# Kernel optimization log

Measured on AMD Instinct MI355X. Metric: run time of the kernel, lower is better.

Reference implementation:

```python
import jax, jax.numpy as jnp
import numpy as np

B = 1024
D = 64          # embed_dim (symp == dise)
H1, H2 = 8, 8   # dsd metapath fanouts
U1, U2, U3 = 8, 8, 16  # usu metapath fanouts
NUM_SYMP = 50000
NUM_DISE = 2000
NEG_SLOPE = 0.2


def setup_inputs() -> dict:
    key = jax.random.key(0)
    ks = jax.random.split(key, 16)
    s = 0.05
    E_s = jax.random.normal(ks[0], (NUM_SYMP + 1, D), jnp.float32) * s
    E_d = jax.random.normal(ks[1], (NUM_DISE + 1, D), jnp.float32) * s
    # padding_idx=0 rows are zero in torch Embedding
    E_s = E_s.at[0].set(0.0)
    E_d = E_d.at[0].set(0.0)
    W = lambda k: jax.random.normal(k, (D, D), jnp.float32) * (1.0 / np.sqrt(D))
    return {
        "E_s": E_s,
        "E_d": E_d,
        "W_dsd_21": W(ks[2]),
        "W_dsd_22": W(ks[3]),
        "W_dsd_11": W(ks[4]),
        "W_dsd_12": W(ks[5]),
        "W_usu_3": W(ks[6]),
        "W_usu_21": W(ks[7]),
        "W_usu_22": W(ks[8]),
        "W_usu_1": W(ks[9]),
        "label": jax.random.randint(ks[10], (B,), 0, NUM_DISE + 1),
        "dsd_1": jax.random.randint(ks[11], (B, H1), 0, NUM_SYMP + 1),
        "dsd_2": jax.random.randint(ks[12], (B, H1, H2), 0, NUM_DISE + 1),
        "usu_1": jax.random.randint(ks[13], (B, U1), 0, NUM_SYMP + 1),
        "usu_2": jax.random.randint(ks[14], (B, U1, U2), 0, 10000),
        "usu_3": jax.random.randint(ks[15], (B, U1, U2, U3), 0, NUM_SYMP + 1),
    }


def _avg_real(msg, idx):
    # mean over the neighbor axis, counting only nonzero (real) neighbors;
    # zero output if all neighbors are padding (matches weight==1e8 -> 0)
    cnt = (idx != 0).sum(-1).astype(msg.dtype)
    w = jnp.where(cnt > 0, 1.0 / (cnt + 1e-8), 0.0)
    return msg.sum(-2) * w[..., None]


def _leaky(x):
    return jax.nn.leaky_relu(x, NEG_SLOPE)


def reference(E_s, E_d, W_dsd_21, W_dsd_22, W_dsd_11, W_dsd_12,
              W_usu_3, W_usu_21, W_usu_22, W_usu_1,
              label, dsd_1, dsd_2, usu_1, usu_2, usu_3):
    # ---- forward_dsd (eval mode: dropout = identity) ----
    td = E_d[label]                       # [B, D]
    es = E_s[dsd_1]                       # [B, H1, D]
    ed = E_d[dsd_2]                       # [B, H1, H2, D]
    m_sd = ed @ W_dsd_21.T + (ed * es[:, :, None, :]) @ W_dsd_22.T
    m_sd = _avg_real(m_sd, dsd_2)         # [B, H1, D]
    m_ss = es @ W_dsd_21.T                # [B, H1, D]
    emb_s1 = _leaky(m_ss + m_sd)          # [B, H1, D]
    m_ds = emb_s1 @ W_dsd_11.T + (emb_s1 * td[:, None, :]) @ W_dsd_12.T
    m_ds = _avg_real(m_ds, dsd_1)         # [B, D]
    emb_dise = _leaky(m_ds + td @ W_dsd_11.T)

    # ---- forward_usu ----
    u1 = E_s[usu_1]                       # [B, U1, D]
    s3 = E_s[usu_3]                       # [B, U1, U2, U3, D]
    m_us3 = _avg_real(s3 @ W_usu_3.T, usu_3)   # [B, U1, U2, D]
    eu2 = _leaky(m_us3)                   # [B, U1, U2, D]
    m_su = eu2 @ W_usu_21.T + (eu2 * u1[:, :, None, :]) @ W_usu_22.T
    m_su = _avg_real(m_su, usu_2)         # [B, U1, D]
    m_ss_u = u1 @ W_usu_21.T              # [B, U1, D]
    es1 = _leaky(m_ss_u + m_su)           # [B, U1, D]
    emb_user = _leaky(_avg_real(es1 @ W_usu_1.T, usu_1))  # [B, D]

    pred_score = (emb_dise * emb_user).sum(-1)  # [B]
    return pred_score
```

## Files before the change

kernel.cpp:

```cpp
#include <hip/hip_runtime.h>
#include <hip/hip_bf16.h>


typedef __attribute__((ext_vector_type(8))) short short8;
typedef __attribute__((ext_vector_type(8))) unsigned short ushort8;
typedef __attribute__((ext_vector_type(4))) float f32x4;

__device__ __forceinline__ int rfl(int v) { return __builtin_amdgcn_readfirstlane(v); }
__device__ __forceinline__ float bcastf(float v, int l) {
    return __int_as_float(__builtin_amdgcn_readlane(__float_as_int(v), l));
}
__device__ __forceinline__ float leakyf(float x) { return x >= 0.f ? x : 0.2f * x; }

__device__ __forceinline__ unsigned short bf16bits(float x) {
    __hip_bfloat16 h = __float2bfloat16(x);
    return __builtin_bit_cast(unsigned short, h);
}
__device__ __forceinline__ float bflo(unsigned int u) { return __uint_as_float(u << 16); }
__device__ __forceinline__ float bfhi(unsigned int u) { return __uint_as_float(u & 0xffff0000u); }

__device__ __forceinline__ void stage_w512(float* dst, const float* __restrict__ W, int tid) {
#pragma unroll
    for (int c = 0; c < 2; ++c) {
        int f4 = c * 512 + tid;
        int j = f4 >> 4, g = f4 & 15;
        float4 v = reinterpret_cast<const float4*>(W)[f4];
        reinterpret_cast<float4*>(dst)[(j << 4) + ((g + j) & 15)] = v;
    }
}

__device__ __forceinline__ float dot1_lds(float x, const float* w, int lane) {
    float a0 = 0.f, a1 = 0.f, a2 = 0.f, a3 = 0.f;
#pragma unroll
    for (int g = 0; g < 16; ++g) {
        float4 c = reinterpret_cast<const float4*>(w)[(lane << 4) + ((g + lane) & 15)];
        int k = 4 * g;
        a0 = fmaf(bcastf(x, k + 0), c.x, a0);
        a1 = fmaf(bcastf(x, k + 1), c.y, a1);
        a2 = fmaf(bcastf(x, k + 2), c.z, a2);
        a3 = fmaf(bcastf(x, k + 3), c.w, a3);
    }
    return (a0 + a1) + (a2 + a3);
}

__global__ __launch_bounds__(256) void k_cvt(const float* __restrict__ E_s,
                                             unsigned short* __restrict__ T) {
    int t = blockIdx.x * 256 + threadIdx.x;
    if (t >= 400008) return;
    const float4* p = reinterpret_cast<const float4*>(E_s) + (size_t)t * 2;
    float4 a = p[0], b = p[1];
    ushort8 o;
    o[0] = bf16bits(a.x); o[1] = bf16bits(a.y); o[2] = bf16bits(a.z); o[3] = bf16bits(a.w);
    o[4] = bf16bits(b.x); o[5] = bf16bits(b.y); o[6] = bf16bits(b.z); o[7] = bf16bits(b.w);
    *(reinterpret_cast<ushort8*>(T) + t) = o;
}

#define XP 72

__device__ __forceinline__ f32x4 pair_mfma(
    const unsigned short* sXs, const unsigned short* sXm,
    const unsigned short* sWb1, const unsigned short* sWb2,
    int arow, int brow, int quad)
{
    const int ab = arow * XP + quad * 8;
    const int bb = brow * XP + quad * 8;
    short8 as0 = *(const short8*)(sXs + ab);
    short8 as1 = *(const short8*)(sXs + ab + 32);
    short8 am0 = *(const short8*)(sXm + ab);
    short8 am1 = *(const short8*)(sXm + ab + 32);
    short8 b10 = *(const short8*)(sWb1 + bb);
    short8 b11 = *(const short8*)(sWb1 + bb + 32);
    short8 b20 = *(const short8*)(sWb2 + bb);
    short8 b21 = *(const short8*)(sWb2 + bb + 32);
    f32x4 acc = {0.f, 0.f, 0.f, 0.f};
    acc = __builtin_amdgcn_mfma_f32_16x16x32_bf16(as0, b10, acc, 0, 0, 0);
    acc = __builtin_amdgcn_mfma_f32_16x16x32_bf16(as1, b11, acc, 0, 0, 0);
    acc = __builtin_amdgcn_mfma_f32_16x16x32_bf16(am0, b20, acc, 0, 0, 0);
    acc = __builtin_amdgcn_mfma_f32_16x16x32_bf16(am1, b21, acc, 0, 0, 0);
    return acc;
}

__global__ __launch_bounds__(512, 4) void k_main(
    const float* __restrict__ E_s, const unsigned short* __restrict__ Ebf,
    const float* __restrict__ E_d,
    const float* __restrict__ W21, const float* __restrict__ W22,
    const float* __restrict__ W11, const float* __restrict__ W12,
    const float* __restrict__ W3, const float* __restrict__ W21u,
    const float* __restrict__ W22u, const float* __restrict__ W1u,
    const int* __restrict__ label, const int* __restrict__ dsd_1,
    const int* __restrict__ dsd_2, const int* __restrict__ usu_1,
    const int* __restrict__ usu_2, const int* __restrict__ usu_3,
    float* __restrict__ emb_dise, float* __restrict__ emb_user)
{
    __shared__ float4 smraw[2560];
    const int tid = threadIdx.x, lane = tid & 63, w = rfl(tid >> 6);
    const int m_ = lane & 15, quad = lane >> 4;

    if (blockIdx.x < 1024) {
        const int b = blockIdx.x;
        unsigned short* sXb   = (unsigned short*)smraw;
        unsigned short* sW3b  = sXb + 4608;
        unsigned short* sW21b = sW3b + 4608;
        unsigned short* sW22b = sW21b + 4608;
        float* sA2  = (float*)(sW22b + 4608);
        float* sES1 = sA2 + 512;
        unsigned short* sXs = sXb;
        unsigned short* sXm = sXb + 16 * XP;

        const int sub = lane >> 4, cg = lane & 15;

        int idv[8];
#pragma unroll
        for (int i = 0; i < 8; ++i)
            idv[i] = usu_3[((size_t)(b * 64 + w * 8 + i)) * 16 + cg];

        {
            int row = tid >> 3, c0 = (tid & 7) << 3;
            const float* p3 = W3 + row * 64 + c0;
            const float* p1 = W21u + row * 64 + c0;
            const float* p2 = W22u + row * 64 + c0;
#pragma unroll
            for (int i = 0; i < 8; ++i) {
                sW3b[row * XP + c0 + i]  = bf16bits(p3[i]);
                sW21b[row * XP + c0 + i] = bf16bits(p1[i]);
                sW22b[row * XP + c0 + i] = bf16bits(p2[i]);
            }
        }

        uint2 vbuf[32];
#pragma unroll
        for (int i = 0; i < 8; ++i) {
#pragma unroll
            for (int k = 0; k < 4; ++k) {
                int id = __shfl(idv[i], k * 4 + sub, 64);
                vbuf[i * 4 + k] =
                    *reinterpret_cast<const uint2*>(Ebf + (size_t)id * 64 + cg * 4);
            }
        }
#pragma unroll
        for (int i = 0; i < 8; ++i) {
            int ql = w * 8 + i;
            unsigned long long nzm = __ballot(idv[i] != 0) & 0xFFFFull;
            int cnt = (int)__popcll(nzm);
            float wgt = cnt > 0 ? 1.f / ((float)cnt + 1e-8f) : 0.f;
            float a0 = 0.f, a1 = 0.f, a2 = 0.f, a3 = 0.f;
#pragma unroll
            for (int k = 0; k < 4; ++k) {
                uint2 v = vbuf[i * 4 + k];
                a0 += bflo(v.x); a1 += bfhi(v.x);
                a2 += bflo(v.y); a3 += bfhi(v.y);
            }
            a0 += __shfl_xor(a0, 16, 64); a1 += __shfl_xor(a1, 16, 64);
            a2 += __shfl_xor(a2, 16, 64); a3 += __shfl_xor(a3, 16, 64);
            a0 += __shfl_xor(a0, 32, 64); a1 += __shfl_xor(a1, 32, 64);
            a2 += __shfl_xor(a2, 32, 64); a3 += __shfl_xor(a3, 32, 64);
            a0 *= wgt; a1 *= wgt; a2 *= wgt; a3 *= wgt;
            unsigned int p0 = ((unsigned int)bf16bits(a1) << 16) | bf16bits(a0);
            unsigned int p1 = ((unsigned int)bf16bits(a3) << 16) | bf16bits(a2);
            if (sub == 0) {
                uint2 st; st.x = p0; st.y = p1;
                *reinterpret_cast<uint2*>(sXb + ql * XP + cg * 4) = st;
            }
        }
        __syncthreads();

        {
            const int wt = w >> 1, J0 = (w & 1) * 2;
            const int base = (16 * wt + m_) * XP + quad * 8;
            short8 a0 = *(const short8*)(sXb + base);
            short8 a1 = *(const short8*)(sXb + base + 32);
            int cp0 = 0, cp1 = 0;
            const int* m2 = usu_2 + (b * 8 + 2 * wt) * 8;
#pragma unroll
            for (int u = 0; u < 8; ++u) { cp0 += (m2[u] != 0); cp1 += (m2[u + 8] != 0); }
            float wg0 = cp0 > 0 ? 1.f / ((float)cp0 + 1e-8f) : 0.f;
            float wg1 = cp1 > 0 ? 1.f / ((float)cp1 + 1e-8f) : 0.f;
#pragma unroll
            for (int jj = 0; jj < 2; ++jj) {
                int J = J0 + jj;
                const int wb = (16 * J + m_) * XP + quad * 8;
                short8 b0 = *(const short8*)(sW3b + wb);
                short8 b1 = *(const short8*)(sW3b + wb + 32);
                f32x4 acc = {0.f, 0.f, 0.f, 0.f};
                acc = __builtin_amdgcn_mfma_f32_16x16x32_bf16(a0, b0, acc, 0, 0, 0);
                acc = __builtin_amdgcn_mfma_f32_16x16x32_bf16(a1, b1, acc, 0, 0, 0);
                float t = leakyf(acc[0]) + leakyf(acc[1]) + leakyf(acc[2]) + leakyf(acc[3]);
                t += __shfl_xor(t, 16, 64);
                if (quad == 0) sA2[(2 * wt + 0) * 64 + J * 16 + m_] = t * wg0;
                if (quad == 2) sA2[(2 * wt + 1) * 64 + J * 16 + m_] = t * wg1;
            }
        }
        __syncthreads();

        {
            int p = w;
            float x = sA2[p * 64 + lane];
            float u1e = E_s[(size_t)usu_1[b * 8 + p] * 64 + lane];
            sXs[p * XP + lane] = bf16bits(x + u1e);
            sXm[p * XP + lane] = bf16bits(x * u1e);
        }
        __syncthreads();

        if (w < 4) {
            f32x4 acc = pair_mfma(sXs, sXm, sW21b, sW22b, m_, 16 * w + m_, quad);
            if (quad < 2) {
#pragma unroll
                for (int r = 0; r < 4; ++r)
                    sES1[(quad * 4 + r) * 64 + w * 16 + m_] = leakyf(acc[r]);
            }
        }
        __syncthreads();

        stage_w512((float*)sW21b, W1u, tid);
        __syncthreads();

        if (w == 0) {
            float sE = 0.f; int cnt = 0;
            const int* u1i = usu_1 + b * 8;
#pragma unroll
            for (int h = 0; h < 8; ++h) {
                sE += sES1[h * 64 + lane];
                cnt += (u1i[h] != 0);
            }
            float wgt = cnt > 0 ? 1.f / ((float)cnt + 1e-8f) : 0.f;
            float eu = leakyf(dot1_lds(sE * wgt, (float*)sW21b, lane));
            emb_user[(size_t)b * 64 + lane] = eu;
        }
    } else {
        const int b0 = (blockIdx.x - 1024) * 4;
        unsigned short* sXs   = (unsigned short*)smraw;
        unsigned short* sXm   = sXs + 2304;
        unsigned short* sW21b = sXm + 2304;
        unsigned short* sW22b = sW21b + 4608;
        float* sS1 = (float*)(sW22b + 4608);

        {
            int row = tid >> 3, c0 = (tid & 7) << 3;
            const float* p1 = W21 + row * 64 + c0;
            const float* p2 = W22 + row * 64 + c0;
#pragma unroll
            for (int i = 0; i < 8; ++i) {
                sW21b[row * XP + c0 + i] = bf16bits(p1[i]);
                sW22b[row * XP + c0 + i] = bf16bits(p2[i]);
            }
        }

#pragma unroll
        for (int i = 0; i < 4; ++i) {
            int rl = w * 4 + i;
            int row = b0 * 8 + rl;
            int is = dsd_1[row];
            float es = E_s[(size_t)is * 64 + lane];
            const int* d2 = dsd_2 + row * 8;
            float sA = 0.f; int cnt = 0;
#pragma unroll
            for (int h = 0; h < 8; ++h) {
                int id = d2[h];
                cnt += (id != 0);
                sA += E_d[(size_t)id * 64 + lane];
            }
            float wgt = cnt > 0 ? 1.f / ((float)cnt + 1e-8f) : 0.f;
            float A = sA * wgt;
            sXs[rl * XP + lane] = bf16bits(A + es);
            sXm[rl * XP + lane] = bf16bits(A * es);
        }
        __syncthreads();

        {
            const int Mt = w >> 2, J = w & 3;
            f32x4 acc = pair_mfma(sXs, sXm, sW21b, sW22b,
                                  16 * Mt + m_, 16 * J + m_, quad);
#pragma unroll
            for (int r = 0; r < 4; ++r)
                sS1[(16 * Mt + quad * 4 + r) * 64 + J * 16 + m_] = leakyf(acc[r]);
        }
        __syncthreads();

        if (w < 4) {
            int bb = b0 + w;
            float sE = 0.f; int cnt = 0;
            const int* d1 = dsd_1 + bb * 8;
#pragma unroll
            for (int h = 0; h < 8; ++h) {
                sE += sS1[(w * 8 + h) * 64 + lane];
                cnt += (d1[h] != 0);
            }
            float wgt = cnt > 0 ? 1.f / ((float)cnt + 1e-8f) : 0.f;
            float A3 = sE * wgt;
            float td = E_d[(size_t)label[bb] * 64 + lane];
            sXs[w * XP + lane] = bf16bits(A3 + td);
            sXm[w * XP + lane] = bf16bits(A3 * td);
        } else {
            int t2 = tid - 256;
            int row = t2 >> 2, c0 = (t2 & 3) << 4;
            const float* p1 = W11 + row * 64 + c0;
            const float* p2 = W12 + row * 64 + c0;
#pragma unroll
            for (int i = 0; i < 16; ++i) {
                sW21b[row * XP + c0 + i] = bf16bits(p1[i]);
                sW22b[row * XP + c0 + i] = bf16bits(p2[i]);
            }
        }
        __syncthreads();

        if (w < 4) {
            f32x4 acc = pair_mfma(sXs, sXm, sW21b, sW22b, m_, 16 * w + m_, quad);
            if (quad == 0) {
#pragma unroll
                for (int r = 0; r < 4; ++r)
                    emb_dise[(size_t)(b0 + r) * 64 + w * 16 + m_] = leakyf(acc[r]);
            }
        }
    }
}

__global__ __launch_bounds__(256) void k_dot(const float* __restrict__ ed,
                                             const float* __restrict__ eu,
                                             float* __restrict__ out) {
    const int lane = threadIdx.x & 63;
    const int b = rfl((int)((blockIdx.x * blockDim.x + threadIdx.x) >> 6));
    float pr = ed[(size_t)b * 64 + lane] * eu[(size_t)b * 64 + lane];
#pragma unroll
    for (int off = 32; off > 0; off >>= 1) pr += __shfl_down(pr, off, 64);
    if (lane == 0) out[b] = pr;
}

extern "C" void kernel_launch(void* const* d_in, const int* in_sizes, int n_in,
                              void* d_out, int out_size, void* d_ws, size_t ws_size,
                              hipStream_t stream) {
    const float* E_s  = (const float*)d_in[0];
    const float* E_d  = (const float*)d_in[1];
    const float* W_dsd_21 = (const float*)d_in[2];
    const float* W_dsd_22 = (const float*)d_in[3];
    const float* W_dsd_11 = (const float*)d_in[4];
    const float* W_dsd_12 = (const float*)d_in[5];
    const float* W_usu_3  = (const float*)d_in[6];
    const float* W_usu_21 = (const float*)d_in[7];
    const float* W_usu_22 = (const float*)d_in[8];
    const float* W_usu_1  = (const float*)d_in[9];
    const int* label = (const int*)d_in[10];
    const int* dsd_1 = (const int*)d_in[11];
    const int* dsd_2 = (const int*)d_in[12];
    const int* usu_1 = (const int*)d_in[13];
    const int* usu_2 = (const int*)d_in[14];
    const int* usu_3 = (const int*)d_in[15];
    float* out = (float*)d_out;

    unsigned short* Ebf = (unsigned short*)d_ws;
    float* emb_dise = (float*)((char*)d_ws + 6400128);
    float* emb_user = emb_dise + 1024 * 64;

    k_cvt<<<1563, 256, 0, stream>>>(E_s, Ebf);
    k_main<<<1280, 512, 0, stream>>>(E_s, Ebf, E_d,
                                     W_dsd_21, W_dsd_22, W_dsd_11, W_dsd_12,
                                     W_usu_3, W_usu_21, W_usu_22, W_usu_1,
                                     label, dsd_1, dsd_2, usu_1, usu_2, usu_3,
                                     emb_dise, emb_user);
    k_dot<<<256, 256, 0, stream>>>(emb_dise, emb_user, out);
}
```

Baseline: 119.8 us.

## Split usu_3 gather-and-average into separate kernel to cut k_main register pressure

Moves the 16-neighbour bf16 embedding gather and masked mean for usu_3 out of k_main into a new k_gather kernel that writes averaged rows to a workspace buffer. k_main then loads those rows with one vector load per thread, which frees its 32-entry vbuf register array, and its launch bound is raised to 6 blocks per SM for higher occupancy. The trade-off is an extra kernel launch plus a round trip of the intermediate through global memory.

```diff
diff --git a/kernel.cpp b/kernel.cpp
--- a/kernel.cpp
+++ b/kernel.cpp
@@ -53,6 +53,54 @@
     o[0] = bf16bits(a.x); o[1] = bf16bits(a.y); o[2] = bf16bits(a.z); o[3] = bf16bits(a.w);
     o[4] = bf16bits(b.x); o[5] = bf16bits(b.y); o[6] = bf16bits(b.z); o[7] = bf16bits(b.w);
     *(reinterpret_cast<ushort8*>(T) + t) = o;
+}
+
+__global__ __launch_bounds__(256, 6) void k_gather(
+    const unsigned short* __restrict__ Ebf,
+    const int* __restrict__ usu_3,
+    unsigned short* __restrict__ Xbuf)
+{
+    const int tid = threadIdx.x, lane = tid & 63;
+    const int wv = (blockIdx.x << 2) + (tid >> 6);
+    const int g0 = wv << 2;
+    const int sub = lane >> 4, cg = lane & 15;
+
+    int idv = usu_3[g0 * 16 + lane];
+    unsigned long long nz = __ballot(idv != 0);
+
+    uint2 vb[16];
+#pragma unroll
+    for (int q = 0; q < 4; ++q) {
+#pragma unroll
+        for (int k = 0; k < 4; ++k) {
+            int id = __shfl(idv, q * 16 + k * 4 + sub, 64);
+            vb[q * 4 + k] =
+                *reinterpret_cast<const uint2*>(Ebf + (size_t)id * 64 + cg * 4);
+        }
+    }
+#pragma unroll
+    for (int q = 0; q < 4; ++q) {
+        int cnt = (int)__popcll((nz >> (q * 16)) & 0xFFFFull);
+        float wgt = cnt > 0 ? 1.f / ((float)cnt + 1e-8f) : 0.f;
+        float a0 = 0.f, a1 = 0.f, a2 = 0.f, a3 = 0.f;
+#pragma unroll
+        for (int k = 0; k < 4; ++k) {
+            uint2 v = vb[q * 4 + k];
+            a0 += bflo(v.x); a1 += bfhi(v.x);
+            a2 += bflo(v.y); a3 += bfhi(v.y);
+        }
+        a0 += __shfl_xor(a0, 16, 64); a1 += __shfl_xor(a1, 16, 64);
+        a2 += __shfl_xor(a2, 16, 64); a3 += __shfl_xor(a3, 16, 64);
+        a0 += __shfl_xor(a0, 32, 64); a1 += __shfl_xor(a1, 32, 64);
+        a2 += __shfl_xor(a2, 32, 64); a3 += __shfl_xor(a3, 32, 64);
+        a0 *= wgt; a1 *= wgt; a2 *= wgt; a3 *= wgt;
+        if (sub == 0) {
+            unsigned int p0 = ((unsigned int)bf16bits(a1) << 16) | bf16bits(a0);
+            unsigned int p1 = ((unsigned int)bf16bits(a3) << 16) | bf16bits(a2);
+            uint2 st; st.x = p0; st.y = p1;
+            *reinterpret_cast<uint2*>(Xbuf + (size_t)(g0 + q) * 64 + cg * 4) = st;
+        }
+    }
 }
 
 #define XP 72
@@ -80,9 +128,9 @@
     return acc;
 }
 
-__global__ __launch_bounds__(512, 4) void k_main(
+__global__ __launch_bounds__(512, 6) void k_main(
     const float* __restrict__ E_s, const unsigned short* __restrict__ Ebf,
-    const float* __restrict__ E_d,
+    const float* __restrict__ E_d, const unsigned short* __restrict__ Xbuf,
     const float* __restrict__ W21, const float* __restrict__ W22,
     const float* __restrict__ W11, const float* __restrict__ W12,
     const float* __restrict__ W3, const float* __restrict__ W21u,
@@ -107,12 +155,12 @@
         unsigned short* sXs = sXb;
         unsigned short* sXm = sXb + 16 * XP;
 
-        const int sub = lane >> 4, cg = lane & 15;
-
-        int idv[8];
-#pragma unroll
-        for (int i = 0; i < 8; ++i)
-            idv[i] = usu_3[((size_t)(b * 64 + w * 8 + i)) * 16 + cg];
+        {
+            int row = tid >> 3, c0 = (tid & 7) << 3;
+            uint4 v = *reinterpret_cast<const uint4*>(
+                Xbuf + (size_t)(b * 64 + row) * 64 + c0);
+            *reinterpret_cast<uint4*>(sXb + row * XP + c0) = v;
+        }
 
         {
             int row = tid >> 3, c0 = (tid & 7) << 3;
@@ -124,42 +172,6 @@
                 sW3b[row * XP + c0 + i]  = bf16bits(p3[i]);
                 sW21b[row * XP + c0 + i] = bf16bits(p1[i]);
                 sW22b[row * XP + c0 + i] = bf16bits(p2[i]);
-            }
-        }
-
-        uint2 vbuf[32];
-#pragma unroll
-        for (int i = 0; i < 8; ++i) {
-#pragma unroll
-            for (int k = 0; k < 4; ++k) {
-                int id = __shfl(idv[i], k * 4 + sub, 64);
-                vbuf[i * 4 + k] =
-                    *reinterpret_cast<const uint2*>(Ebf + (size_t)id * 64 + cg * 4);
-            }
-        }
-#pragma unroll
-        for (int i = 0; i < 8; ++i) {
-            int ql = w * 8 + i;
-            unsigned long long nzm = __ballot(idv[i] != 0) & 0xFFFFull;
-            int cnt = (int)__popcll(nzm);
-            float wgt = cnt > 0 ? 1.f / ((float)cnt + 1e-8f) : 0.f;
-            float a0 = 0.f, a1 = 0.f, a2 = 0.f, a3 = 0.f;
-#pragma unroll
-            for (int k = 0; k < 4; ++k) {
-                uint2 v = vbuf[i * 4 + k];
-                a0 += bflo(v.x); a1 += bfhi(v.x);
-                a2 += bflo(v.y); a3 += bfhi(v.y);
-            }
-            a0 += __shfl_xor(a0, 16, 64); a1 += __shfl_xor(a1, 16, 64);
-            a2 += __shfl_xor(a2, 16, 64); a3 += __shfl_xor(a3, 16, 64);
-            a0 += __shfl_xor(a0, 32, 64); a1 += __shfl_xor(a1, 32, 64);
-            a2 += __shfl_xor(a2, 32, 64); a3 += __shfl_xor(a3, 32, 64);
-            a0 *= wgt; a1 *= wgt; a2 *= wgt; a3 *= wgt;
-            unsigned int p0 = ((unsigned int)bf16bits(a1) << 16) | bf16bits(a0);
-            unsigned int p1 = ((unsigned int)bf16bits(a3) << 16) | bf16bits(a2);
-            if (sub == 0) {
-                uint2 st; st.x = p0; st.y = p1;
-                *reinterpret_cast<uint2*>(sXb + ql * XP + cg * 4) = st;
             }
         }
         __syncthreads();
@@ -349,9 +361,11 @@
     unsigned short* Ebf = (unsigned short*)d_ws;
     float* emb_dise = (float*)((char*)d_ws + 6400128);
     float* emb_user = emb_dise + 1024 * 64;
+    unsigned short* Xbuf = (unsigned short*)(emb_user + 1024 * 64);
 
     k_cvt<<<1563, 256, 0, stream>>>(E_s, Ebf);
-    k_main<<<1280, 512, 0, stream>>>(E_s, Ebf, E_d,
+    k_gather<<<4096, 256, 0, stream>>>(Ebf, usu_3, Xbuf);
+    k_main<<<1280, 512, 0, stream>>>(E_s, Ebf, E_d, Xbuf,
                                      W_dsd_21, W_dsd_22, W_dsd_11, W_dsd_12,
                                      W_usu_3, W_usu_21, W_usu_22, W_usu_1,
                                      label, dsd_1, dsd_2, usu_1, usu_2, usu_3,
```

Result: no change. 121.7 us (+1.6%).
